# Kernel optimization log

Hardware: AMD Instinct MI355X
Metric: run time of the kernel (lower is better)

Reference implementation:

```python
import jax, jax.numpy as jnp
import numpy as np

B, N, D = 8, 256, 64  # batch, n_entities, feature dim


def setup_inputs() -> dict:
    key = jax.random.key(0)
    ks = jax.random.split(key, 8)
    s = 0.02
    return {
        "emb1": jax.random.normal(ks[0], (B, N, D), jnp.float32),
        "emb2": jax.random.normal(ks[1], (B, N, N, D), jnp.float32),
        "W1a": jax.random.normal(ks[2], (3 * D, 128), jnp.float32) * s,
        "b1a": jnp.zeros((128,), jnp.float32),
        "W1b": jax.random.normal(ks[3], (128, D), jnp.float32) * s,
        "b1b": jnp.zeros((D,), jnp.float32),
        "W2a": jax.random.normal(ks[4], (4 * D, 256), jnp.float32) * s,
        "b2a": jnp.zeros((256,), jnp.float32),
        "W2b": jax.random.normal(ks[5], (256, D), jnp.float32) * s,
        "b2b": jnp.zeros((D,), jnp.float32),
    }


def _mlp(x, Wa, ba, Wb, bb):
    h = jax.nn.relu(jnp.einsum("...i,io->...o", x, Wa) + ba)
    return jnp.einsum("...i,io->...o", h, Wb) + bb


def reference(emb1, emb2, W1a, b1a, W1b, b1b, W2a, b2a, W2b, b2b):
    # arity 1: reduce arity-2 embedding over second entity dim (max & min), concat
    red_max = jnp.max(emb2, axis=-2)           # [B,N,D]
    red_min = jnp.min(emb2, axis=-2)           # [B,N,D]
    cat1 = jnp.concatenate([emb1, red_max, red_min], axis=-1)  # [B,N,3D]

    # arity 2: expand arity-1 embedding along a new entity dim, concat with emb2
    exp = jnp.broadcast_to(emb1[:, :, None, :], emb2.shape)    # [B,N,N,D]
    cat2 = jnp.concatenate([exp, emb2], axis=-1)               # [B,N,N,2D]

    # permutation gather: position (i,j) gets [cat2[j,i], cat2[i,j]] along features
    perm2 = jnp.concatenate([jnp.transpose(cat2, (0, 2, 1, 3)), cat2], axis=-1)  # [B,N,N,4D]

    out1 = _mlp(cat1, W1a, b1a, W1b, b1b)    # [B,N,D]
    out2 = _mlp(perm2, W2a, b2a, W2b, b2b)   # [B,N,N,D]
    return (out1, out2)
```

## Files before the change

### kernel.cpp

```cpp
#include <hip/hip_runtime.h>
#include <hip/hip_bf16.h>

typedef __bf16 bf16x8 __attribute__((ext_vector_type(8)));
typedef float f32x4 __attribute__((ext_vector_type(4)));
typedef unsigned int u32;
typedef unsigned short u16;
typedef u32 u32x4 __attribute__((ext_vector_type(4)));
typedef u16 u16x4 __attribute__((ext_vector_type(4)));
typedef u16 u16x8 __attribute__((ext_vector_type(8)));

__device__ __forceinline__ u16 f2bf(float x) {
  u32 u = __float_as_uint(x);
  return (u16)((u + 0x7FFFu + ((u >> 16) & 1u)) >> 16);
}

__device__ __forceinline__ bf16x8 ld_frag_lds(const u16* base, int byteOff) {
  u32x4 v = *(const u32x4*)((const char*)base + byteOff);
  return __builtin_bit_cast(bf16x8, v);
}

__device__ __forceinline__ bf16x8 ld_frag_glb(const u16* p) {
  u32x4 v = *(const u32x4*)p;
  return __builtin_bit_cast(bf16x8, v);
}

__global__ void prep_kernel(const float* __restrict__ W2a, const float* __restrict__ W2b,
                            u16* __restrict__ wfA, u16* __restrict__ wfB) {
  int t = blockIdx.x * 256 + threadIdx.x;
  if (t < 8192) {
    int lane = t & 63;
    int ks = (t >> 6) & 7;
    int ntg = t >> 9;
    int col = (ntg << 4) + (lane & 15);
    int kb = (ks << 5) + ((lane >> 4) << 3);
#pragma unroll
    for (int q = 0; q < 8; ++q)
      wfA[t * 8 + q] = f2bf(W2a[(kb + q) * 256 + col]);
  } else if (t < 10240) {
    int t2 = t - 8192;
    int lane = t2 & 63;
    int ks = (t2 >> 6) & 7;
    int ntg = t2 >> 9;
    int col = (ntg << 4) + (lane & 15);
    int kb = (ks << 5) + ((lane >> 4) << 3);
#pragma unroll
    for (int q = 0; q < 8; ++q)
      wfB[t2 * 8 + q] = f2bf(W2b[(kb + q) * 64 + col]);
  }
}

__global__ __launch_bounds__(256, 2) void fused_kernel(
    const float* __restrict__ emb1, const float* __restrict__ emb2,
    const float* __restrict__ W1a, const float* __restrict__ b1a,
    const float* __restrict__ W1b, const float* __restrict__ b1b,
    const float* __restrict__ b2a, const float* __restrict__ b2b,
    const u16* __restrict__ wfA, const u16* __restrict__ wfB,
    float* __restrict__ out1, float* __restrict__ out2) {
  __shared__ __align__(16) u16 S[64 * 256];

  int blk = blockIdx.x;
  int t = threadIdx.x;

  if (blk >= 8192) {
    int bi = blk - 8192;
    float* f = (float*)S;
    float* smax = f;
    float* smin = f + 256;
    float* cat1 = f + 512;
    float* h    = f + 704;

    int d = t & 63, q = t >> 6;
    const float* base = emb2 + (size_t)bi * 256 * 64;
    float vmax = -INFINITY, vmin = INFINITY;
    for (int j = q; j < 256; j += 4) {
      float v = base[j * 64 + d];
      vmax = fmaxf(vmax, v);
      vmin = fminf(vmin, v);
    }
    smax[q * 64 + d] = vmax;
    smin[q * 64 + d] = vmin;
    __syncthreads();
    if (t < 64) {
      float mx = fmaxf(fmaxf(smax[t], smax[64 + t]), fmaxf(smax[128 + t], smax[192 + t]));
      float mn = fminf(fminf(smin[t], smin[64 + t]), fminf(smin[128 + t], smin[192 + t]));
      cat1[t] = emb1[bi * 64 + t];
      cat1[64 + t] = mx;
      cat1[128 + t] = mn;
    }
    __syncthreads();
    if (t < 128) {
      float acc = b1a[t];
      for (int k = 0; k < 192; ++k) acc += cat1[k] * W1a[k * 128 + t];
      h[t] = fmaxf(acc, 0.f);
    }
    __syncthreads();
    if (t < 64) {
      float acc = b1b[t];
      for (int k = 0; k < 128; ++k) acc += h[k] * W1b[k * 64 + t];
      out1[bi * 64 + t] = acc;
    }
    return;
  }

  int b = blk >> 10;
  int i = (blk >> 2) & 255;
  int j0 = (blk & 3) << 6;
  int lane = t & 63;
  int w = t >> 6;
  int lr = lane & 15;
  int lg = lane >> 4;

  {
    int r = t >> 2;
    int c16 = (t & 3) << 4;
    const float* s0 = emb1 + ((b << 8) + j0 + r) * 64;
    const float* s1 = emb2 + ((((size_t)(b << 8) + j0 + r) << 8) + i) * 64;
    const float* s2 = emb1 + ((b << 8) + i) * 64;
    const float* s3 = emb2 + ((((size_t)(b << 8) + i) << 8) + (j0 + r)) * 64;
    const float* srcs[4] = {s0, s1, s2, s3};
#pragma unroll
    for (int seg = 0; seg < 4; ++seg) {
      const float* src = srcs[seg];
#pragma unroll
      for (int u = 0; u < 2; ++u) {
        int d = c16 + (u << 3);
        float4 v0 = *(const float4*)(src + d);
        float4 v1 = *(const float4*)(src + d + 4);
        u16x8 o = {f2bf(v0.x), f2bf(v0.y), f2bf(v0.z), f2bf(v0.w),
                   f2bf(v1.x), f2bf(v1.y), f2bf(v1.z), f2bf(v1.w)};
        int byteOff = (r * 512 + ((seg << 6) + d) * 2) ^ ((r & 7) << 4);
        *(u16x8*)((char*)S + byteOff) = o;
      }
    }
  }
  __syncthreads();

  f32x4 acc1[4][4];
#pragma unroll
  for (int m = 0; m < 4; ++m)
#pragma unroll
    for (int nt = 0; nt < 4; ++nt) acc1[m][nt] = (f32x4){0.f, 0.f, 0.f, 0.f};

#pragma unroll
  for (int ks = 0; ks < 8; ++ks) {
    int kByte = (ks << 6) + (lg << 4);
    bf16x8 a[4];
#pragma unroll
    for (int m = 0; m < 4; ++m) {
      int r = (m << 4) + lr;
      int off = (r * 512 + kByte) ^ ((r & 7) << 4);
      a[m] = ld_frag_lds(S, off);
    }
    bf16x8 bw[4];
#pragma unroll
    for (int nt = 0; nt < 4; ++nt)
      bw[nt] = ld_frag_glb(wfA + (size_t)((((w << 2) + nt) * 8 + ks) * 64 + lane) * 8);
#pragma unroll
    for (int m = 0; m < 4; ++m)
#pragma unroll
      for (int nt = 0; nt < 4; ++nt)
        acc1[m][nt] = __builtin_amdgcn_mfma_f32_16x16x32_bf16(bw[nt], a[m], acc1[m][nt], 0, 0, 0);
  }

  __syncthreads();

#pragma unroll
  for (int nt = 0; nt < 4; ++nt) {
    float4 bias4 = *(const float4*)(b2a + (w << 6) + (nt << 4) + (lg << 2));
#pragma unroll
    for (int m = 0; m < 4; ++m) {
      int j = (m << 4) + lr;
      u16x4 o = {f2bf(fmaxf(acc1[m][nt][0] + bias4.x, 0.f)),
                 f2bf(fmaxf(acc1[m][nt][1] + bias4.y, 0.f)),
                 f2bf(fmaxf(acc1[m][nt][2] + bias4.z, 0.f)),
                 f2bf(fmaxf(acc1[m][nt][3] + bias4.w, 0.f))};
      int nByte = ((w << 6) + (nt << 4) + (lg << 2)) * 2;
      int off = (j * 512 + nByte) ^ ((j & 7) << 4);
      *(u16x4*)((char*)S + off) = o;
    }
  }
  __syncthreads();

  f32x4 acc2[4];
#pragma unroll
  for (int jt = 0; jt < 4; ++jt) acc2[jt] = (f32x4){0.f, 0.f, 0.f, 0.f};

#pragma unroll
  for (int ks = 0; ks < 8; ++ks) {
    int kByte = (ks << 6) + (lg << 4);
    bf16x8 bwB = ld_frag_glb(wfB + (size_t)(((w << 3) + ks) * 64 + lane) * 8);
#pragma unroll
    for (int jt = 0; jt < 4; ++jt) {
      int j = (jt << 4) + lr;
      int off = (j * 512 + kByte) ^ ((j & 7) << 4);
      bf16x8 h = ld_frag_lds(S, off);
      acc2[jt] = __builtin_amdgcn_mfma_f32_16x16x32_bf16(bwB, h, acc2[jt], 0, 0, 0);
    }
  }

  float4 bias2 = *(const float4*)(b2b + (w << 4) + (lg << 2));
  float* obase = out2 + ((((size_t)(b << 8) + i) << 8) + j0) * 64 + (w << 4) + (lg << 2);
#pragma unroll
  for (int jt = 0; jt < 4; ++jt) {
    float4 v = {acc2[jt][0] + bias2.x, acc2[jt][1] + bias2.y,
                acc2[jt][2] + bias2.z, acc2[jt][3] + bias2.w};
    *(float4*)(obase + (size_t)((jt << 4) + lr) * 64) = v;
  }
}

extern "C" void kernel_launch(void* const* d_in, const int* in_sizes, int n_in,
                              void* d_out, int out_size, void* d_ws, size_t ws_size,
                              hipStream_t stream) {
  const float* emb1 = (const float*)d_in[0];
  const float* emb2 = (const float*)d_in[1];
  const float* W1a  = (const float*)d_in[2];
  const float* b1a  = (const float*)d_in[3];
  const float* W1b  = (const float*)d_in[4];
  const float* b1b  = (const float*)d_in[5];
  const float* W2a  = (const float*)d_in[6];
  const float* b2a  = (const float*)d_in[7];
  const float* W2b  = (const float*)d_in[8];
  const float* b2b  = (const float*)d_in[9];

  float* out = (float*)d_out;
  u16* wfA = (u16*)d_ws;
  u16* wfB = wfA + 16 * 8 * 64 * 8;

  prep_kernel<<<40, 256, 0, stream>>>(W2a, W2b, wfA, wfB);
  fused_kernel<<<10240, 256, 0, stream>>>(emb1, emb2, W1a, b1a, W1b, b1b,
                                          b2a, b2b, wfA, wfB,
                                          out, out + 8 * 256 * 64);
}
```

Baseline: 187.0 us.

## Precompute emb1 contributions of first MLP layer per entity, halve GEMM K

```diff
diff --git a/kernel.cpp b/kernel.cpp
--- a/kernel.cpp
+++ b/kernel.cpp
@@ -14,6 +14,11 @@
   return (u16)((u + 0x7FFFu + ((u >> 16) & 1u)) >> 16);
 }
 
+__device__ __forceinline__ u16 cvt_bf16(float x) {
+  __bf16 h = (__bf16)x;
+  return __builtin_bit_cast(u16, h);
+}
+
 __device__ __forceinline__ bf16x8 ld_frag_lds(const u16* base, int byteOff) {
   u32x4 v = *(const u32x4*)((const char*)base + byteOff);
   return __builtin_bit_cast(bf16x8, v);
@@ -24,46 +29,68 @@
   return __builtin_bit_cast(bf16x8, v);
 }
 
-__global__ void prep_kernel(const float* __restrict__ W2a, const float* __restrict__ W2b,
-                            u16* __restrict__ wfA, u16* __restrict__ wfB) {
+__global__ void prep_w_kernel(const float* __restrict__ W2a, const float* __restrict__ W2b,
+                              u16* __restrict__ wfA, u16* __restrict__ wfB) {
   int t = blockIdx.x * 256 + threadIdx.x;
-  if (t < 8192) {
+  if (t < 4096) {
     int lane = t & 63;
-    int ks = (t >> 6) & 7;
-    int ntg = t >> 9;
+    int ks = (t >> 6) & 3;
+    int ntg = t >> 8;
     int col = (ntg << 4) + (lane & 15);
-    int kb = (ks << 5) + ((lane >> 4) << 3);
+    int k = (ks << 5) + ((lane >> 4) << 3);
+    int row = (k < 64) ? (64 + k) : (128 + k);
 #pragma unroll
     for (int q = 0; q < 8; ++q)
-      wfA[t * 8 + q] = f2bf(W2a[(kb + q) * 256 + col]);
-  } else if (t < 10240) {
-    int t2 = t - 8192;
+      wfA[t * 8 + q] = f2bf(W2a[(row + q) * 256 + col]);
+  } else if (t < 6144) {
+    int t2 = t - 4096;
     int lane = t2 & 63;
     int ks = (t2 >> 6) & 7;
     int ntg = t2 >> 9;
     int col = (ntg << 4) + (lane & 15);
-    int kb = (ks << 5) + ((lane >> 4) << 3);
+    int k = (ks << 5) + ((lane >> 4) << 3);
 #pragma unroll
     for (int q = 0; q < 8; ++q)
-      wfB[t2 * 8 + q] = f2bf(W2b[(kb + q) * 64 + col]);
-  }
+      wfB[t2 * 8 + q] = f2bf(W2b[(k + q) * 64 + col]);
+  }
+}
+
+__global__ __launch_bounds__(256) void prep_T_kernel(
+    const float* __restrict__ emb1, const float* __restrict__ W2a,
+    const float* __restrict__ b2a, float* __restrict__ T0, float* __restrict__ T2) {
+  __shared__ float e1row[64];
+  int bn = blockIdx.x;
+  int t = threadIdx.x;
+  if (t < 64) e1row[t] = emb1[bn * 64 + t];
+  __syncthreads();
+  float a0 = b2a[t];
+  float a2 = 0.f;
+#pragma unroll 8
+  for (int k = 0; k < 64; ++k) {
+    float e = e1row[k];
+    a0 += e * W2a[k * 256 + t];
+    a2 += e * W2a[(128 + k) * 256 + t];
+  }
+  T0[(size_t)bn * 256 + t] = a0;
+  T2[(size_t)bn * 256 + t] = a2;
 }
 
 __global__ __launch_bounds__(256, 2) void fused_kernel(
     const float* __restrict__ emb1, const float* __restrict__ emb2,
     const float* __restrict__ W1a, const float* __restrict__ b1a,
     const float* __restrict__ W1b, const float* __restrict__ b1b,
-    const float* __restrict__ b2a, const float* __restrict__ b2b,
+    const float* __restrict__ b2b,
     const u16* __restrict__ wfA, const u16* __restrict__ wfB,
+    const float* __restrict__ T0, const float* __restrict__ T2,
     float* __restrict__ out1, float* __restrict__ out2) {
-  __shared__ __align__(16) u16 S[64 * 256];
+  __shared__ __align__(16) u16 SH[24576];
 
   int blk = blockIdx.x;
   int t = threadIdx.x;
 
   if (blk >= 8192) {
     int bi = blk - 8192;
-    float* f = (float*)S;
+    float* f = (float*)SH;
     float* smax = f;
     float* smin = f + 256;
     float* cat1 = f + 512;
@@ -110,27 +137,27 @@
   int lr = lane & 15;
   int lg = lane >> 4;
 
+  const u16* X = SH;
+  const u16* H = SH + 8192;
+  char* Xb = (char*)SH;
+  char* Hb = (char*)SH + 16384;
+
   {
     int r = t >> 2;
-    int c16 = (t & 3) << 4;
-    const float* s0 = emb1 + ((b << 8) + j0 + r) * 64;
-    const float* s1 = emb2 + ((((size_t)(b << 8) + j0 + r) << 8) + i) * 64;
-    const float* s2 = emb1 + ((b << 8) + i) * 64;
-    const float* s3 = emb2 + ((((size_t)(b << 8) + i) << 8) + (j0 + r)) * 64;
-    const float* srcs[4] = {s0, s1, s2, s3};
-#pragma unroll
-    for (int seg = 0; seg < 4; ++seg) {
-      const float* src = srcs[seg];
-#pragma unroll
-      for (int u = 0; u < 2; ++u) {
-        int d = c16 + (u << 3);
-        float4 v0 = *(const float4*)(src + d);
-        float4 v1 = *(const float4*)(src + d + 4);
-        u16x8 o = {f2bf(v0.x), f2bf(v0.y), f2bf(v0.z), f2bf(v0.w),
-                   f2bf(v1.x), f2bf(v1.y), f2bf(v1.z), f2bf(v1.w)};
-        int byteOff = (r * 512 + ((seg << 6) + d) * 2) ^ ((r & 7) << 4);
-        *(u16x8*)((char*)S + byteOff) = o;
-      }
+    int q = t & 3;
+    const float* s1 = emb2 + (((size_t)b * 256 + (j0 + r)) * 256 + i) * 64;
+    const float* s3 = emb2 + (((size_t)b * 256 + i) * 256 + (j0 + r)) * 64;
+    const float* src = (q < 2) ? (s1 + (q << 5)) : (s3 + ((q - 2) << 5));
+    float4 v[8];
+#pragma unroll
+    for (int u = 0; u < 8; ++u) v[u] = *(const float4*)(src + (u << 2));
+#pragma unroll
+    for (int u = 0; u < 4; ++u) {
+      float4 a0 = v[u * 2], a1 = v[u * 2 + 1];
+      u16x8 o = {cvt_bf16(a0.x), cvt_bf16(a0.y), cvt_bf16(a0.z), cvt_bf16(a0.w),
+                 cvt_bf16(a1.x), cvt_bf16(a1.y), cvt_bf16(a1.z), cvt_bf16(a1.w)};
+      int off = (r * 256 + (q << 6) + (u << 4)) ^ ((r & 7) << 4);
+      *(u16x8*)(Xb + off) = o;
     }
   }
   __syncthreads();
@@ -142,19 +169,18 @@
     for (int nt = 0; nt < 4; ++nt) acc1[m][nt] = (f32x4){0.f, 0.f, 0.f, 0.f};
 
 #pragma unroll
-  for (int ks = 0; ks < 8; ++ks) {
+  for (int ks = 0; ks < 4; ++ks) {
     int kByte = (ks << 6) + (lg << 4);
     bf16x8 a[4];
 #pragma unroll
     for (int m = 0; m < 4; ++m) {
-      int r = (m << 4) + lr;
-      int off = (r * 512 + kByte) ^ ((r & 7) << 4);
-      a[m] = ld_frag_lds(S, off);
+      int off = (((m << 4) + lr) * 256 + kByte) ^ ((lr & 7) << 4);
+      a[m] = ld_frag_lds(X, off);
     }
     bf16x8 bw[4];
 #pragma unroll
     for (int nt = 0; nt < 4; ++nt)
-      bw[nt] = ld_frag_glb(wfA + (size_t)((((w << 2) + nt) * 8 + ks) * 64 + lane) * 8);
+      bw[nt] = ld_frag_glb(wfA + (size_t)((((w << 2) + nt) * 4 + ks) * 64 + lane) * 8);
 #pragma unroll
     for (int m = 0; m < 4; ++m)
 #pragma unroll
@@ -162,21 +188,20 @@
         acc1[m][nt] = __builtin_amdgcn_mfma_f32_16x16x32_bf16(bw[nt], a[m], acc1[m][nt], 0, 0, 0);
   }
 
-  __syncthreads();
-
 #pragma unroll
   for (int nt = 0; nt < 4; ++nt) {
-    float4 bias4 = *(const float4*)(b2a + (w << 6) + (nt << 4) + (lg << 2));
+    int n_lo = (((w << 2) + nt) << 4) + (lg << 2);
+    float4 t2v = *(const float4*)(T2 + ((size_t)b * 256 + i) * 256 + n_lo);
 #pragma unroll
     for (int m = 0; m < 4; ++m) {
-      int j = (m << 4) + lr;
-      u16x4 o = {f2bf(fmaxf(acc1[m][nt][0] + bias4.x, 0.f)),
-                 f2bf(fmaxf(acc1[m][nt][1] + bias4.y, 0.f)),
-                 f2bf(fmaxf(acc1[m][nt][2] + bias4.z, 0.f)),
-                 f2bf(fmaxf(acc1[m][nt][3] + bias4.w, 0.f))};
-      int nByte = ((w << 6) + (nt << 4) + (lg << 2)) * 2;
-      int off = (j * 512 + nByte) ^ ((j & 7) << 4);
-      *(u16x4*)((char*)S + off) = o;
+      int jrow = (m << 4) + lr;
+      float4 t0v = *(const float4*)(T0 + ((size_t)b * 256 + j0 + jrow) * 256 + n_lo);
+      u16x4 o = {cvt_bf16(fmaxf(acc1[m][nt][0] + t0v.x + t2v.x, 0.f)),
+                 cvt_bf16(fmaxf(acc1[m][nt][1] + t0v.y + t2v.y, 0.f)),
+                 cvt_bf16(fmaxf(acc1[m][nt][2] + t0v.z + t2v.z, 0.f)),
+                 cvt_bf16(fmaxf(acc1[m][nt][3] + t0v.w + t2v.w, 0.f))};
+      int off = (jrow * 512 + n_lo * 2) ^ ((lr & 7) << 4);
+      *(u16x4*)(Hb + off) = o;
     }
   }
   __syncthreads();
@@ -191,15 +216,14 @@
     bf16x8 bwB = ld_frag_glb(wfB + (size_t)(((w << 3) + ks) * 64 + lane) * 8);
 #pragma unroll
     for (int jt = 0; jt < 4; ++jt) {
-      int j = (jt << 4) + lr;
-      int off = (j * 512 + kByte) ^ ((j & 7) << 4);
-      bf16x8 h = ld_frag_lds(S, off);
+      int off = (((jt << 4) + lr) * 512 + kByte) ^ ((lr & 7) << 4);
+      bf16x8 h = ld_frag_lds(H, off);
       acc2[jt] = __builtin_amdgcn_mfma_f32_16x16x32_bf16(bwB, h, acc2[jt], 0, 0, 0);
     }
   }
 
   float4 bias2 = *(const float4*)(b2b + (w << 4) + (lg << 2));
-  float* obase = out2 + ((((size_t)(b << 8) + i) << 8) + j0) * 64 + (w << 4) + (lg << 2);
+  float* obase = out2 + (((size_t)b * 256 + i) * 256 + j0) * 64 + (w << 4) + (lg << 2);
 #pragma unroll
   for (int jt = 0; jt < 4; ++jt) {
     float4 v = {acc2[jt][0] + bias2.x, acc2[jt][1] + bias2.y,
@@ -224,10 +248,13 @@
 
   float* out = (float*)d_out;
   u16* wfA = (u16*)d_ws;
-  u16* wfB = wfA + 16 * 8 * 64 * 8;
-
-  prep_kernel<<<40, 256, 0, stream>>>(W2a, W2b, wfA, wfB);
+  u16* wfB = wfA + 32768;
+  float* T0 = (float*)(wfB + 16384);
+  float* T2 = T0 + 8 * 256 * 256;
+
+  prep_w_kernel<<<24, 256, 0, stream>>>(W2a, W2b, wfA, wfB);
+  prep_T_kernel<<<2048, 256, 0, stream>>>(emb1, W2a, b2a, T0, T2);
   fused_kernel<<<10240, 256, 0, stream>>>(emb1, emb2, W1a, b1a, W1b, b1b,
-                                          b2a, b2b, wfA, wfB,
+                                          b2b, wfA, wfB, T0, T2,
                                           out, out + 8 * 256 * 64);
 }
```

After: 216.3 us. 1.16x slower.
